# Kernel optimization log

Hardware: AMD Instinct MI355X
Metric: run time of the kernel (lower is better)

The kernel has to match this reference:

```python
import jax, jax.numpy as jnp
import numpy as np

B, D, H, W, C = 4, 128, 128, 128, 16  # batch, feature_dim, height, width, n_classes


def setup_inputs() -> dict:
    key = jax.random.key(0)
    k1, k2, k3 = jax.random.split(key, 3)
    batch_x = jax.random.normal(k1, (B, D, H, W), dtype=jnp.float32)
    # labels in [1, C] (class 0 and 17 are excluded by the original module)
    batch_label = jax.random.randint(k2, (B, H, W), 1, C + 1, dtype=jnp.int32)
    batch_mask = jax.random.randint(k3, (B, 1, H, W), 0, 2, dtype=jnp.int32)
    return {"batch_x": batch_x, "batch_label": batch_label, "batch_mask": batch_mask}


def reference(batch_x, batch_label, batch_mask):
    # local (0-based) class ids
    local = batch_label - 1                                     # [B,H,W]
    onehot = jax.nn.one_hot(local, C, dtype=batch_x.dtype)      # [B,H,W,C]
    counts = onehot.sum(axis=(1, 2))                            # [B,C]
    # per-class prototype = mean of features over pixels with that label
    protos = jnp.einsum('bdhw,bhwc->bcd', batch_x, onehot) / counts[:, :, None]  # [B,C,D]
    # L1 metric: pd0[b,c,h,w] = exp(-sum_d |x[b,d,h,w] - proto[b,c,d]|)
    pd0 = jnp.exp(-jnp.sum(jnp.abs(batch_x[:, None, :, :, :] - protos[:, :, :, None, None]), axis=2))  # [B,C,H,W]
    pd = pd0 - jnp.min(pd0, axis=1, keepdims=True)              # shift (softmax-invariant, kept for fidelity)
    # per-pixel cross-entropy with pd as logits
    logp = jax.nn.log_softmax(pd, axis=1)                       # [B,C,H,W]
    ce = -jnp.take_along_axis(logp, local[:, None, :, :], axis=1)[:, 0]  # [B,H,W]
    m = batch_mask[:, 0].astype(batch_x.dtype)                  # [B,H,W]
    per_sample = (ce * m).sum(axis=(1, 2)) / m.sum(axis=(1, 2))
    # original: total_loss += per-sample masked-mean loss; final divide by x.shape[0]==1
    return per_sample.sum()
```

## Files before the change

kernel.cpp:

```cpp
#include <hip/hip_runtime.h>

constexpr int Bn = 4, Dn = 128, Hn = 128, Wn = 128, Cn = 16;
constexpr int NPIX = Hn * Wn;
constexpr int PS = 2;
constexpr int CS = 8;


__global__ __launch_bounds__(256) void k_proto(
        const float* __restrict__ x,
        const int* __restrict__ label,
        const int* __restrict__ mask,
        float* __restrict__ protoPart,
        float* __restrict__ countsPart,
        float* __restrict__ maskPart) {
    int bid = blockIdx.x;
    int chunk = bid & (PS - 1);
    int d = (bid >> 1) & (Dn - 1);
    int b = bid >> 8;
    int tid = threadIdx.x;
    int wid = tid >> 6, lane = tid & 63;

    constexpr int CH = NPIX / PS;
    const float4* xp = (const float4*)(x + (size_t)(b * Dn + d) * NPIX + chunk * CH);
    const int4*   lp = (const int4*)(label + (size_t)b * NPIX + chunk * CH);

    float acc[Cn];
#pragma unroll
    for (int c = 0; c < Cn; ++c) acc[c] = 0.f;

#pragma unroll 4
    for (int i = tid; i < CH / 4; i += 256) {
        float4 xv = xp[i];
        int4 lv = lp[i];
        int l0 = lv.x - 1, l1 = lv.y - 1, l2 = lv.z - 1, l3 = lv.w - 1;
#pragma unroll
        for (int c = 0; c < Cn; ++c) {
            acc[c] += ((l0 == c) ? xv.x : 0.f) + ((l1 == c) ? xv.y : 0.f)
                    + ((l2 == c) ? xv.z : 0.f) + ((l3 == c) ? xv.w : 0.f);
        }
    }

#pragma unroll
    for (int c = 0; c < Cn; ++c)
        for (int off = 32; off; off >>= 1) acc[c] += __shfl_down(acc[c], off);

    __shared__ float red[4][Cn];
    if (lane == 0) {
#pragma unroll
        for (int c = 0; c < Cn; ++c) red[wid][c] = acc[c];
    }
    __syncthreads();
    if (tid < Cn) {
        float s = red[0][tid] + red[1][tid] + red[2][tid] + red[3][tid];
        protoPart[(((size_t)(b * PS + chunk)) * Dn + d) * Cn + tid] = s;
    }

    if (d < 4) {
        int s = chunk * 4 + d;
        const int4* lp2 = (const int4*)(label + (size_t)b * NPIX + s * 2048);
        const int4* mp2 = (const int4*)(mask  + (size_t)b * NPIX + s * 2048);
        int cnt[Cn];
#pragma unroll
        for (int c = 0; c < Cn; ++c) cnt[c] = 0;
        int msum = 0;
        for (int i = tid; i < 512; i += 256) {
            int4 lv = lp2[i];
            int4 mv = mp2[i];
            msum += mv.x + mv.y + mv.z + mv.w;
            int l0 = lv.x - 1, l1 = lv.y - 1, l2 = lv.z - 1, l3 = lv.w - 1;
#pragma unroll
            for (int c = 0; c < Cn; ++c) {
                cnt[c] += (int)__popcll(__ballot(l0 == c))
                        + (int)__popcll(__ballot(l1 == c))
                        + (int)__popcll(__ballot(l2 == c))
                        + (int)__popcll(__ballot(l3 == c));
            }
        }
        for (int off = 32; off; off >>= 1) msum += __shfl_down(msum, off);

        __shared__ int redi[4][Cn + 1];
        if (lane == 0) {
#pragma unroll
            for (int c = 0; c < Cn; ++c) redi[wid][c] = cnt[c];
            redi[wid][Cn] = msum;
        }
        __syncthreads();
        if (tid < Cn) {
            int t = redi[0][tid] + redi[1][tid] + redi[2][tid] + redi[3][tid];
            countsPart[((size_t)b * CS + s) * Cn + tid] = (float)t;
        } else if (tid == Cn) {
            int t = redi[0][Cn] + redi[1][Cn] + redi[2][Cn] + redi[3][Cn];
            maskPart[b * CS + s] = (float)t;
        }
    }
}

__global__ __launch_bounds__(256, 4) void k_main(
        const float* __restrict__ x,
        const int* __restrict__ label,
        const int* __restrict__ mask,
        const float* __restrict__ protoPart,
        const float* __restrict__ countsPart,
        float* __restrict__ cePart) {
    int b = blockIdx.x >> 7;
    int pbase = (blockIdx.x & 127) << 7;
    int tid = threadIdx.x;
    int lx = tid & 63, dg = tid >> 6;

    __shared__ float smem[4 * Cn * 128];
    __shared__ float cntInv[Cn];
    __shared__ float r2[2];
    float (*proto)[Cn] = (float (*)[Cn])smem;
    float (*part)[Cn][128] = (float (*)[Cn][128])smem;

    if (tid < Cn) {
        float s = 0.f;
#pragma unroll
        for (int q = 0; q < CS; ++q)
            s += countsPart[((size_t)b * CS + q) * Cn + tid];
        cntInv[tid] = 1.f / s;
    }
    __syncthreads();

    const float* pp0 = protoPart + ((size_t)(b * PS + 0)) * Dn * Cn;
    const float* pp1 = protoPart + ((size_t)(b * PS + 1)) * Dn * Cn;
    for (int i = tid; i < Dn * Cn; i += 256) {
        int c = i & (Cn - 1);
        smem[i] = (pp0[i] + pp1[i]) * cntInv[c];
    }
    __syncthreads();

    float2 acc[Cn];
#pragma unroll
    for (int c = 0; c < Cn; ++c) acc[c] = make_float2(0.f, 0.f);

    const float2* xp = (const float2*)(x + (size_t)b * Dn * NPIX + pbase) + lx;
#pragma unroll 2
    for (int dd = 0; dd < 32; ++dd) {
        int d = (dg << 5) + dd;
        float2 xv = xp[(size_t)d * (NPIX / 2)];
        float4 q0 = *(const float4*)&proto[d][0];
        float4 q1 = *(const float4*)&proto[d][4];
        float4 q2 = *(const float4*)&proto[d][8];
        float4 q3 = *(const float4*)&proto[d][12];
        acc[0].x  += fabsf(xv.x - q0.x);  acc[0].y  += fabsf(xv.y - q0.x);
        acc[1].x  += fabsf(xv.x - q0.y);  acc[1].y  += fabsf(xv.y - q0.y);
        acc[2].x  += fabsf(xv.x - q0.z);  acc[2].y  += fabsf(xv.y - q0.z);
        acc[3].x  += fabsf(xv.x - q0.w);  acc[3].y  += fabsf(xv.y - q0.w);
        acc[4].x  += fabsf(xv.x - q1.x);  acc[4].y  += fabsf(xv.y - q1.x);
        acc[5].x  += fabsf(xv.x - q1.y);  acc[5].y  += fabsf(xv.y - q1.y);
        acc[6].x  += fabsf(xv.x - q1.z);  acc[6].y  += fabsf(xv.y - q1.z);
        acc[7].x  += fabsf(xv.x - q1.w);  acc[7].y  += fabsf(xv.y - q1.w);
        acc[8].x  += fabsf(xv.x - q2.x);  acc[8].y  += fabsf(xv.y - q2.x);
        acc[9].x  += fabsf(xv.x - q2.y);  acc[9].y  += fabsf(xv.y - q2.y);
        acc[10].x += fabsf(xv.x - q2.z);  acc[10].y += fabsf(xv.y - q2.z);
        acc[11].x += fabsf(xv.x - q2.w);  acc[11].y += fabsf(xv.y - q2.w);
        acc[12].x += fabsf(xv.x - q3.x);  acc[12].y += fabsf(xv.y - q3.x);
        acc[13].x += fabsf(xv.x - q3.y);  acc[13].y += fabsf(xv.y - q3.y);
        acc[14].x += fabsf(xv.x - q3.z);  acc[14].y += fabsf(xv.y - q3.z);
        acc[15].x += fabsf(xv.x - q3.w);  acc[15].y += fabsf(xv.y - q3.w);
    }

    __syncthreads();

#pragma unroll
    for (int c = 0; c < Cn; ++c)
        *(float2*)&part[dg][c][lx * 2] = acc[c];
    __syncthreads();

    float v = 0.f;
    if (tid < 128) {
        float a[Cn];
#pragma unroll
        for (int c = 0; c < Cn; ++c)
            a[c] = part[0][c][tid] + part[1][c][tid]
                 + part[2][c][tid] + part[3][c][tid];

        float pd0[Cn];
        float mn = 3.4e38f;
#pragma unroll
        for (int c = 0; c < Cn; ++c) {
            pd0[c] = __expf(-a[c]);
            mn = fminf(mn, pd0[c]);
        }
        float se = 0.f;
#pragma unroll
        for (int c = 0; c < Cn; ++c) se += __expf(pd0[c] - mn);

        int p = pbase + tid;
        int l = label[b * NPIX + p] - 1;
        float pdl = 0.f;
#pragma unroll
        for (int c = 0; c < Cn; ++c) pdl = (l == c) ? (pd0[c] - mn) : pdl;

        float ce = __logf(se) - pdl;
        float m = (float)mask[b * NPIX + p];
        v = ce * m;

        for (int off = 32; off; off >>= 1) v += __shfl_down(v, off);
        if ((tid & 63) == 0) r2[tid >> 6] = v;
    }
    __syncthreads();
    if (tid == 0) cePart[blockIdx.x] = r2[0] + r2[1];
}

__global__ void k_final(const float* __restrict__ cePart,
                        const float* __restrict__ maskPart,
                        float* __restrict__ out) {
    int tid = threadIdx.x;
    int w = tid >> 6, lane = tid & 63;

    float s = cePart[w * 128 + lane] + cePart[w * 128 + lane + 64];
    for (int off = 32; off; off >>= 1) s += __shfl_down(s, off);

    __shared__ float r[4];
    if (lane == 0) {
        float ms = 0.f;
#pragma unroll
        for (int q = 0; q < CS; ++q) ms += maskPart[w * CS + q];
        r[w] = s / ms;
    }
    __syncthreads();
    if (tid == 0) out[0] = r[0] + r[1] + r[2] + r[3];
}

extern "C" void kernel_launch(void* const* d_in, const int* in_sizes, int n_in,
                              void* d_out, int out_size, void* d_ws, size_t ws_size,
                              hipStream_t stream) {
    const float* x     = (const float*)d_in[0];
    const int*   label = (const int*)d_in[1];
    const int*   mask  = (const int*)d_in[2];
    float* out = (float*)d_out;

    float* ws         = (float*)d_ws;
    float* protoPart  = ws;
    float* countsPart = protoPart + Bn * PS * Dn * Cn;
    float* maskPart   = countsPart + Bn * CS * Cn;
    float* cePart     = maskPart + Bn * CS;

    k_proto<<<Bn * Dn * PS, 256, 0, stream>>>(x, label, mask,
                                              protoPart, countsPart, maskPart);
    k_main <<<Bn * (NPIX / 128), 256, 0, stream>>>(x, label, mask,
                                                   protoPart, countsPart, cePart);
    k_final<<<1, 256, 0, stream>>>(cePart, maskPart, out);
}
```

Before: 39.52 us.

## Drop final kernel via atomics, read unnormalised proto sums from global in main

The prototype kernel now runs one 512-thread block per (batch, feature) instead of splitting pixels in two, so it writes full sums with no partial merge. The main kernel no longer stages normalised prototypes in shared memory. It reads the raw sums directly from global memory, computes |cnt*x - S| with an FMA, and scales by 1/count after the reduction. The separate final kernel is removed: each main block atomically adds its mask-normalised partial loss to the output, which the first kernel zeroes. This saves a launch and a shared-memory staging pass, at the cost of non-deterministic atomic ordering and per-iteration global/scalar loads of the prototype rows.

Measured after the change: 43.75 us. 10.7% more time.

```diff
diff --git a/kernel.cpp b/kernel.cpp
--- a/kernel.cpp
+++ b/kernel.cpp
@@ -2,34 +2,34 @@
 
 constexpr int Bn = 4, Dn = 128, Hn = 128, Wn = 128, Cn = 16;
 constexpr int NPIX = Hn * Wn;
-constexpr int PS = 2;
 constexpr int CS = 8;
 
 
-__global__ __launch_bounds__(256) void k_proto(
+__global__ __launch_bounds__(512) void k_proto(
         const float* __restrict__ x,
         const int* __restrict__ label,
         const int* __restrict__ mask,
-        float* __restrict__ protoPart,
+        float* __restrict__ protoSum,
         float* __restrict__ countsPart,
-        float* __restrict__ maskPart) {
+        float* __restrict__ maskPart,
+        float* __restrict__ out) {
     int bid = blockIdx.x;
-    int chunk = bid & (PS - 1);
-    int d = (bid >> 1) & (Dn - 1);
-    int b = bid >> 8;
+    int d = bid & (Dn - 1);
+    int b = bid >> 7;
     int tid = threadIdx.x;
     int wid = tid >> 6, lane = tid & 63;
 
-    constexpr int CH = NPIX / PS;
-    const float4* xp = (const float4*)(x + (size_t)(b * Dn + d) * NPIX + chunk * CH);
-    const int4*   lp = (const int4*)(label + (size_t)b * NPIX + chunk * CH);
+    if (bid == 0 && tid == 0) out[0] = 0.f;
+
+    const float4* xp = (const float4*)(x + (size_t)bid * NPIX);
+    const int4*   lp = (const int4*)(label + (size_t)b * NPIX);
 
     float acc[Cn];
 #pragma unroll
     for (int c = 0; c < Cn; ++c) acc[c] = 0.f;
 
 #pragma unroll 4
-    for (int i = tid; i < CH / 4; i += 256) {
+    for (int i = tid; i < NPIX / 4; i += 512) {
         float4 xv = xp[i];
         int4 lv = lp[i];
         int l0 = lv.x - 1, l1 = lv.y - 1, l2 = lv.z - 1, l3 = lv.w - 1;
@@ -44,41 +44,39 @@
     for (int c = 0; c < Cn; ++c)
         for (int off = 32; off; off >>= 1) acc[c] += __shfl_down(acc[c], off);
 
-    __shared__ float red[4][Cn];
+    __shared__ float red[8][Cn];
     if (lane == 0) {
 #pragma unroll
         for (int c = 0; c < Cn; ++c) red[wid][c] = acc[c];
     }
     __syncthreads();
     if (tid < Cn) {
-        float s = red[0][tid] + red[1][tid] + red[2][tid] + red[3][tid];
-        protoPart[(((size_t)(b * PS + chunk)) * Dn + d) * Cn + tid] = s;
-    }
-
-    if (d < 4) {
-        int s = chunk * 4 + d;
-        const int4* lp2 = (const int4*)(label + (size_t)b * NPIX + s * 2048);
-        const int4* mp2 = (const int4*)(mask  + (size_t)b * NPIX + s * 2048);
+        float s = 0.f;
+#pragma unroll
+        for (int w = 0; w < 8; ++w) s += red[w][tid];
+        protoSum[(size_t)bid * Cn + tid] = s;
+    }
+
+    if (d < CS) {
+        const int4* lp2 = (const int4*)(label + (size_t)b * NPIX + d * 2048);
+        const int4* mp2 = (const int4*)(mask  + (size_t)b * NPIX + d * 2048);
         int cnt[Cn];
 #pragma unroll
         for (int c = 0; c < Cn; ++c) cnt[c] = 0;
-        int msum = 0;
-        for (int i = tid; i < 512; i += 256) {
-            int4 lv = lp2[i];
-            int4 mv = mp2[i];
-            msum += mv.x + mv.y + mv.z + mv.w;
-            int l0 = lv.x - 1, l1 = lv.y - 1, l2 = lv.z - 1, l3 = lv.w - 1;
-#pragma unroll
-            for (int c = 0; c < Cn; ++c) {
-                cnt[c] += (int)__popcll(__ballot(l0 == c))
-                        + (int)__popcll(__ballot(l1 == c))
-                        + (int)__popcll(__ballot(l2 == c))
-                        + (int)__popcll(__ballot(l3 == c));
-            }
+        int4 lv = lp2[tid];
+        int4 mv = mp2[tid];
+        int msum = mv.x + mv.y + mv.z + mv.w;
+        int l0 = lv.x - 1, l1 = lv.y - 1, l2 = lv.z - 1, l3 = lv.w - 1;
+#pragma unroll
+        for (int c = 0; c < Cn; ++c) {
+            cnt[c] += (int)__popcll(__ballot(l0 == c))
+                    + (int)__popcll(__ballot(l1 == c))
+                    + (int)__popcll(__ballot(l2 == c))
+                    + (int)__popcll(__ballot(l3 == c));
         }
         for (int off = 32; off; off >>= 1) msum += __shfl_down(msum, off);
 
-        __shared__ int redi[4][Cn + 1];
+        __shared__ int redi[8][Cn + 1];
         if (lane == 0) {
 #pragma unroll
             for (int c = 0; c < Cn; ++c) redi[wid][c] = cnt[c];
@@ -86,86 +84,109 @@
         }
         __syncthreads();
         if (tid < Cn) {
-            int t = redi[0][tid] + redi[1][tid] + redi[2][tid] + redi[3][tid];
-            countsPart[((size_t)b * CS + s) * Cn + tid] = (float)t;
+            int s = 0;
+#pragma unroll
+            for (int w = 0; w < 8; ++w) s += redi[w][tid];
+            countsPart[((size_t)b * CS + d) * Cn + tid] = (float)s;
         } else if (tid == Cn) {
-            int t = redi[0][Cn] + redi[1][Cn] + redi[2][Cn] + redi[3][Cn];
-            maskPart[b * CS + s] = (float)t;
+            int s = 0;
+#pragma unroll
+            for (int w = 0; w < 8; ++w) s += redi[w][Cn];
+            maskPart[b * CS + d] = (float)s;
         }
     }
 }
 
-__global__ __launch_bounds__(256, 4) void k_main(
+__global__ __launch_bounds__(256) void k_main(
         const float* __restrict__ x,
         const int* __restrict__ label,
         const int* __restrict__ mask,
-        const float* __restrict__ protoPart,
+        const float* __restrict__ protoSum,
         const float* __restrict__ countsPart,
-        float* __restrict__ cePart) {
+        const float* __restrict__ maskPart,
+        float* __restrict__ out) {
     int b = blockIdx.x >> 7;
     int pbase = (blockIdx.x & 127) << 7;
     int tid = threadIdx.x;
-    int lx = tid & 63, dg = tid >> 6;
-
-    __shared__ float smem[4 * Cn * 128];
-    __shared__ float cntInv[Cn];
+    int lane = tid & 63, w = tid >> 6;
+    int wu = __builtin_amdgcn_readfirstlane(w);
+
+    __shared__ float part[4][Cn][128];
+    __shared__ float shCnt[Cn], shCntInv[Cn];
+    __shared__ float shInvMask;
     __shared__ float r2[2];
-    float (*proto)[Cn] = (float (*)[Cn])smem;
-    float (*part)[Cn][128] = (float (*)[Cn][128])smem;
 
     if (tid < Cn) {
         float s = 0.f;
 #pragma unroll
         for (int q = 0; q < CS; ++q)
             s += countsPart[((size_t)b * CS + q) * Cn + tid];
-        cntInv[tid] = 1.f / s;
-    }
-    __syncthreads();
-
-    const float* pp0 = protoPart + ((size_t)(b * PS + 0)) * Dn * Cn;
-    const float* pp1 = protoPart + ((size_t)(b * PS + 1)) * Dn * Cn;
-    for (int i = tid; i < Dn * Cn; i += 256) {
-        int c = i & (Cn - 1);
-        smem[i] = (pp0[i] + pp1[i]) * cntInv[c];
-    }
-    __syncthreads();
+        shCnt[tid] = s;
+        shCntInv[tid] = 1.f / s;
+    } else if (tid == Cn) {
+        float ms = 0.f;
+#pragma unroll
+        for (int q = 0; q < CS; ++q) ms += maskPart[b * CS + q];
+        shInvMask = 1.f / ms;
+    }
+    __syncthreads();
+
+    float cntv[Cn];
+#pragma unroll
+    for (int c = 0; c < Cn; ++c) cntv[c] = shCnt[c];
 
     float2 acc[Cn];
 #pragma unroll
     for (int c = 0; c < Cn; ++c) acc[c] = make_float2(0.f, 0.f);
 
-    const float2* xp = (const float2*)(x + (size_t)b * Dn * NPIX + pbase) + lx;
+    const float2* xp = (const float2*)(x + (size_t)b * Dn * NPIX + pbase);
+    const float4* srow = (const float4*)(protoSum + ((size_t)(b * Dn) + (wu << 5)) * Cn);
+
 #pragma unroll 2
     for (int dd = 0; dd < 32; ++dd) {
-        int d = (dg << 5) + dd;
-        float2 xv = xp[(size_t)d * (NPIX / 2)];
-        float4 q0 = *(const float4*)&proto[d][0];
-        float4 q1 = *(const float4*)&proto[d][4];
-        float4 q2 = *(const float4*)&proto[d][8];
-        float4 q3 = *(const float4*)&proto[d][12];
-        acc[0].x  += fabsf(xv.x - q0.x);  acc[0].y  += fabsf(xv.y - q0.x);
-        acc[1].x  += fabsf(xv.x - q0.y);  acc[1].y  += fabsf(xv.y - q0.y);
-        acc[2].x  += fabsf(xv.x - q0.z);  acc[2].y  += fabsf(xv.y - q0.z);
-        acc[3].x  += fabsf(xv.x - q0.w);  acc[3].y  += fabsf(xv.y - q0.w);
-        acc[4].x  += fabsf(xv.x - q1.x);  acc[4].y  += fabsf(xv.y - q1.x);
-        acc[5].x  += fabsf(xv.x - q1.y);  acc[5].y  += fabsf(xv.y - q1.y);
-        acc[6].x  += fabsf(xv.x - q1.z);  acc[6].y  += fabsf(xv.y - q1.z);
-        acc[7].x  += fabsf(xv.x - q1.w);  acc[7].y  += fabsf(xv.y - q1.w);
-        acc[8].x  += fabsf(xv.x - q2.x);  acc[8].y  += fabsf(xv.y - q2.x);
-        acc[9].x  += fabsf(xv.x - q2.y);  acc[9].y  += fabsf(xv.y - q2.y);
-        acc[10].x += fabsf(xv.x - q2.z);  acc[10].y += fabsf(xv.y - q2.z);
-        acc[11].x += fabsf(xv.x - q2.w);  acc[11].y += fabsf(xv.y - q2.w);
-        acc[12].x += fabsf(xv.x - q3.x);  acc[12].y += fabsf(xv.y - q3.x);
-        acc[13].x += fabsf(xv.x - q3.y);  acc[13].y += fabsf(xv.y - q3.y);
-        acc[14].x += fabsf(xv.x - q3.z);  acc[14].y += fabsf(xv.y - q3.z);
-        acc[15].x += fabsf(xv.x - q3.w);  acc[15].y += fabsf(xv.y - q3.w);
-    }
-
-    __syncthreads();
+        float2 xv = xp[(size_t)((wu << 5) + dd) * (NPIX / 2) + lane];
+        float4 S0 = srow[dd * 4 + 0];
+        float4 S1 = srow[dd * 4 + 1];
+        float4 S2 = srow[dd * 4 + 2];
+        float4 S3 = srow[dd * 4 + 3];
+        float t;
+        t = fmaf(cntv[0],  xv.x, -S0.x); acc[0].x  += fabsf(t);
+        t = fmaf(cntv[0],  xv.y, -S0.x); acc[0].y  += fabsf(t);
+        t = fmaf(cntv[1],  xv.x, -S0.y); acc[1].x  += fabsf(t);
+        t = fmaf(cntv[1],  xv.y, -S0.y); acc[1].y  += fabsf(t);
+        t = fmaf(cntv[2],  xv.x, -S0.z); acc[2].x  += fabsf(t);
+        t = fmaf(cntv[2],  xv.y, -S0.z); acc[2].y  += fabsf(t);
+        t = fmaf(cntv[3],  xv.x, -S0.w); acc[3].x  += fabsf(t);
+        t = fmaf(cntv[3],  xv.y, -S0.w); acc[3].y  += fabsf(t);
+        t = fmaf(cntv[4],  xv.x, -S1.x); acc[4].x  += fabsf(t);
+        t = fmaf(cntv[4],  xv.y, -S1.x); acc[4].y  += fabsf(t);
+        t = fmaf(cntv[5],  xv.x, -S1.y); acc[5].x  += fabsf(t);
+        t = fmaf(cntv[5],  xv.y, -S1.y); acc[5].y  += fabsf(t);
+        t = fmaf(cntv[6],  xv.x, -S1.z); acc[6].x  += fabsf(t);
+        t = fmaf(cntv[6],  xv.y, -S1.z); acc[6].y  += fabsf(t);
+        t = fmaf(cntv[7],  xv.x, -S1.w); acc[7].x  += fabsf(t);
+        t = fmaf(cntv[7],  xv.y, -S1.w); acc[7].y  += fabsf(t);
+        t = fmaf(cntv[8],  xv.x, -S2.x); acc[8].x  += fabsf(t);
+        t = fmaf(cntv[8],  xv.y, -S2.x); acc[8].y  += fabsf(t);
+        t = fmaf(cntv[9],  xv.x, -S2.y); acc[9].x  += fabsf(t);
+        t = fmaf(cntv[9],  xv.y, -S2.y); acc[9].y  += fabsf(t);
+        t = fmaf(cntv[10], xv.x, -S2.z); acc[10].x += fabsf(t);
+        t = fmaf(cntv[10], xv.y, -S2.z); acc[10].y += fabsf(t);
+        t = fmaf(cntv[11], xv.x, -S2.w); acc[11].x += fabsf(t);
+        t = fmaf(cntv[11], xv.y, -S2.w); acc[11].y += fabsf(t);
+        t = fmaf(cntv[12], xv.x, -S3.x); acc[12].x += fabsf(t);
+        t = fmaf(cntv[12], xv.y, -S3.x); acc[12].y += fabsf(t);
+        t = fmaf(cntv[13], xv.x, -S3.y); acc[13].x += fabsf(t);
+        t = fmaf(cntv[13], xv.y, -S3.y); acc[13].y += fabsf(t);
+        t = fmaf(cntv[14], xv.x, -S3.z); acc[14].x += fabsf(t);
+        t = fmaf(cntv[14], xv.y, -S3.z); acc[14].y += fabsf(t);
+        t = fmaf(cntv[15], xv.x, -S3.w); acc[15].x += fabsf(t);
+        t = fmaf(cntv[15], xv.y, -S3.w); acc[15].y += fabsf(t);
+    }
 
 #pragma unroll
     for (int c = 0; c < Cn; ++c)
-        *(float2*)&part[dg][c][lx * 2] = acc[c];
+        *(float2*)&part[w][c][lane * 2] = acc[c];
     __syncthreads();
 
     float v = 0.f;
@@ -173,8 +194,8 @@
         float a[Cn];
 #pragma unroll
         for (int c = 0; c < Cn; ++c)
-            a[c] = part[0][c][tid] + part[1][c][tid]
-                 + part[2][c][tid] + part[3][c][tid];
+            a[c] = (part[0][c][tid] + part[1][c][tid]
+                  + part[2][c][tid] + part[3][c][tid]) * shCntInv[c];
 
         float pd0[Cn];
         float mn = 3.4e38f;
@@ -201,27 +222,7 @@
         if ((tid & 63) == 0) r2[tid >> 6] = v;
     }
     __syncthreads();
-    if (tid == 0) cePart[blockIdx.x] = r2[0] + r2[1];
-}
-
-__global__ void k_final(const float* __restrict__ cePart,
-                        const float* __restrict__ maskPart,
-                        float* __restrict__ out) {
-    int tid = threadIdx.x;
-    int w = tid >> 6, lane = tid & 63;
-
-    float s = cePart[w * 128 + lane] + cePart[w * 128 + lane + 64];
-    for (int off = 32; off; off >>= 1) s += __shfl_down(s, off);
-
-    __shared__ float r[4];
-    if (lane == 0) {
-        float ms = 0.f;
-#pragma unroll
-        for (int q = 0; q < CS; ++q) ms += maskPart[w * CS + q];
-        r[w] = s / ms;
-    }
-    __syncthreads();
-    if (tid == 0) out[0] = r[0] + r[1] + r[2] + r[3];
+    if (tid == 0) atomicAdd(out, (r2[0] + r2[1]) * shInvMask);
 }
 
 extern "C" void kernel_launch(void* const* d_in, const int* in_sizes, int n_in,
@@ -233,14 +234,13 @@
     float* out = (float*)d_out;
 
     float* ws         = (float*)d_ws;
-    float* protoPart  = ws;
-    float* countsPart = protoPart + Bn * PS * Dn * Cn;
+    float* protoSum   = ws;
+    float* countsPart = protoSum + Bn * Dn * Cn;
     float* maskPart   = countsPart + Bn * CS * Cn;
-    float* cePart     = maskPart + Bn * CS;
-
-    k_proto<<<Bn * Dn * PS, 256, 0, stream>>>(x, label, mask,
-                                              protoPart, countsPart, maskPart);
+
+    k_proto<<<Bn * Dn, 512, 0, stream>>>(x, label, mask,
+                                         protoSum, countsPart, maskPart, out);
     k_main <<<Bn * (NPIX / 128), 256, 0, stream>>>(x, label, mask,
-                                                   protoPart, countsPart, cePart);
-    k_final<<<1, 256, 0, stream>>>(cePart, maskPart, out);
+                                                   protoSum, countsPart,
+                                                   maskPart, out);
 }
```

## Drop final reduction kernel via atomicAdd and double prototype split

Applied to the files above, without the earlier changes.

Removes the separate k_final launch. k_main now scales its block's masked CE sum by a per-batch inverse mask count and atomically adds it into the output, which k_proto zeroes first. The prototype pass is split into 4 pixel chunks instead of 2, giving twice as many blocks with shorter loops that are now fully unrolled. This saves one kernel launch and its serialization, at the cost of 512 float atomics, a non-deterministic summation order, and k_main having to sum 4 partial prototypes.

Result: no change. 39.78 us (+0.7%).

```diff
diff --git a/kernel.cpp b/kernel.cpp
--- a/kernel.cpp
+++ b/kernel.cpp
@@ -2,7 +2,7 @@
 
 constexpr int Bn = 4, Dn = 128, Hn = 128, Wn = 128, Cn = 16;
 constexpr int NPIX = Hn * Wn;
-constexpr int PS = 2;
+constexpr int PS = 4;
 constexpr int CS = 8;
 
 
@@ -12,13 +12,16 @@
         const int* __restrict__ mask,
         float* __restrict__ protoPart,
         float* __restrict__ countsPart,
-        float* __restrict__ maskPart) {
+        float* __restrict__ maskPart,
+        float* __restrict__ out) {
     int bid = blockIdx.x;
     int chunk = bid & (PS - 1);
-    int d = (bid >> 1) & (Dn - 1);
-    int b = bid >> 8;
+    int d = (bid >> 2) & (Dn - 1);
+    int b = bid >> 9;
     int tid = threadIdx.x;
     int wid = tid >> 6, lane = tid & 63;
+
+    if (bid == 0 && tid == 0) out[0] = 0.f;
 
     constexpr int CH = NPIX / PS;
     const float4* xp = (const float4*)(x + (size_t)(b * Dn + d) * NPIX + chunk * CH);
@@ -28,7 +31,7 @@
 #pragma unroll
     for (int c = 0; c < Cn; ++c) acc[c] = 0.f;
 
-#pragma unroll 4
+#pragma unroll
     for (int i = tid; i < CH / 4; i += 256) {
         float4 xv = xp[i];
         int4 lv = lp[i];
@@ -55,14 +58,15 @@
         protoPart[(((size_t)(b * PS + chunk)) * Dn + d) * Cn + tid] = s;
     }
 
-    if (d < 4) {
-        int s = chunk * 4 + d;
+    if (d < 2) {
+        int s = chunk * 2 + d;
         const int4* lp2 = (const int4*)(label + (size_t)b * NPIX + s * 2048);
         const int4* mp2 = (const int4*)(mask  + (size_t)b * NPIX + s * 2048);
         int cnt[Cn];
 #pragma unroll
         for (int c = 0; c < Cn; ++c) cnt[c] = 0;
         int msum = 0;
+#pragma unroll
         for (int i = tid; i < 512; i += 256) {
             int4 lv = lp2[i];
             int4 mv = mp2[i];
@@ -101,7 +105,8 @@
         const int* __restrict__ mask,
         const float* __restrict__ protoPart,
         const float* __restrict__ countsPart,
-        float* __restrict__ cePart) {
+        const float* __restrict__ maskPart,
+        float* __restrict__ out) {
     int b = blockIdx.x >> 7;
     int pbase = (blockIdx.x & 127) << 7;
     int tid = threadIdx.x;
@@ -109,6 +114,7 @@
 
     __shared__ float smem[4 * Cn * 128];
     __shared__ float cntInv[Cn];
+    __shared__ float shInvMask;
     __shared__ float r2[2];
     float (*proto)[Cn] = (float (*)[Cn])smem;
     float (*part)[Cn][128] = (float (*)[Cn][128])smem;
@@ -119,14 +125,22 @@
         for (int q = 0; q < CS; ++q)
             s += countsPart[((size_t)b * CS + q) * Cn + tid];
         cntInv[tid] = 1.f / s;
-    }
-    __syncthreads();
-
-    const float* pp0 = protoPart + ((size_t)(b * PS + 0)) * Dn * Cn;
-    const float* pp1 = protoPart + ((size_t)(b * PS + 1)) * Dn * Cn;
-    for (int i = tid; i < Dn * Cn; i += 256) {
-        int c = i & (Cn - 1);
-        smem[i] = (pp0[i] + pp1[i]) * cntInv[c];
+    } else if (tid == Cn) {
+        float ms = 0.f;
+#pragma unroll
+        for (int q = 0; q < CS; ++q) ms += maskPart[b * CS + q];
+        shInvMask = 1.f / ms;
+    }
+    __syncthreads();
+
+    {
+        const float* pp = protoPart + (size_t)b * PS * Dn * Cn;
+        for (int i = tid; i < Dn * Cn; i += 256) {
+            int c = i & (Cn - 1);
+            float s = pp[i] + pp[Dn * Cn + i] + pp[2 * Dn * Cn + i]
+                    + pp[3 * Dn * Cn + i];
+            smem[i] = s * cntInv[c];
+        }
     }
     __syncthreads();
 
@@ -201,27 +215,7 @@
         if ((tid & 63) == 0) r2[tid >> 6] = v;
     }
     __syncthreads();
-    if (tid == 0) cePart[blockIdx.x] = r2[0] + r2[1];
-}
-
-__global__ void k_final(const float* __restrict__ cePart,
-                        const float* __restrict__ maskPart,
-                        float* __restrict__ out) {
-    int tid = threadIdx.x;
-    int w = tid >> 6, lane = tid & 63;
-
-    float s = cePart[w * 128 + lane] + cePart[w * 128 + lane + 64];
-    for (int off = 32; off; off >>= 1) s += __shfl_down(s, off);
-
-    __shared__ float r[4];
-    if (lane == 0) {
-        float ms = 0.f;
-#pragma unroll
-        for (int q = 0; q < CS; ++q) ms += maskPart[w * CS + q];
-        r[w] = s / ms;
-    }
-    __syncthreads();
-    if (tid == 0) out[0] = r[0] + r[1] + r[2] + r[3];
+    if (tid == 0) atomicAdd(out, (r2[0] + r2[1]) * shInvMask);
 }
 
 extern "C" void kernel_launch(void* const* d_in, const int* in_sizes, int n_in,
@@ -236,11 +230,9 @@
     float* protoPart  = ws;
     float* countsPart = protoPart + Bn * PS * Dn * Cn;
     float* maskPart   = countsPart + Bn * CS * Cn;
-    float* cePart     = maskPart + Bn * CS;
-
-    k_proto<<<Bn * Dn * PS, 256, 0, stream>>>(x, label, mask,
-                                              protoPart, countsPart, maskPart);
-    k_main <<<Bn * (NPIX / 128), 256, 0, stream>>>(x, label, mask,
-                                                   protoPart, countsPart, cePart);
-    k_final<<<1, 256, 0, stream>>>(cePart, maskPart, out);
+
+    k_proto<<<Bn * Dn * PS, 256, 0, stream>>>(x, label, mask, protoPart,
+                                              countsPart, maskPart, out);
+    k_main <<<Bn * (NPIX / 128), 256, 0, stream>>>(x, label, mask, protoPart,
+                                                   countsPart, maskPart, out);
 }
```
